# Optimization experiments

Hardware: AMD Instinct MI355X
Metric: run time of the kernel (lower is better)

Reference implementation:

```python
import jax, jax.numpy as jnp
import numpy as np

B, S, H, R = 4, 1024, 1024, 32


def setup_inputs() -> dict:
    key = jax.random.key(0)
    k1, k2, k3 = jax.random.split(key, 3)
    hidden_states = jax.random.normal(k1, (B, S, H), dtype=jnp.float32)
    # full cartesian grid of (seq_idx, hidden_idx), as required by the final
    # out.view(B, S, H, 1) reshape in the original module
    n = jnp.arange(S * H, dtype=jnp.int64)
    all_indices = jnp.stack([n // H, n % H], axis=1)  # [S*H, 2]
    # Linear weights, torch layout [out_features, in_features], scaled like kaiming-uniform-ish
    seq_W = jax.random.normal(k2, (R, H), dtype=jnp.float32) / np.sqrt(H)
    hid_W = jax.random.normal(k3, (R, S), dtype=jnp.float32) / np.sqrt(S)
    cp_weight = jnp.ones((1, R), dtype=jnp.float32)  # frozen all-ones CP mixing weight
    return {"hidden_states": hidden_states, "all_indices": all_indices,
            "seq_W": seq_W, "hid_W": hid_W, "cp_weight": cp_weight}


def reference(hidden_states, all_indices, seq_W, hid_W, cp_weight):
    # seq-mode factor: Linear(H -> R) over [B, S, H] -> [B, S, R]
    seq_emb = jnp.einsum('bsh,rh->bsr', hidden_states, seq_W)
    # hidden-mode factor: Linear(S -> R) over transposed [B, H, S] -> [B, H, R]
    hid_emb = jnp.einsum('bsh,rs->bhr', hidden_states, hid_W)
    s_idx = all_indices[:, 0]  # [N]
    h_idx = all_indices[:, 1]  # [N]
    g_seq = seq_emb[:, s_idx, :]  # [B, N, R] gather along seq axis
    g_hid = hid_emb[:, h_idx, :]  # [B, N, R] gather along hidden axis
    # hadamard + rank reduction with (frozen) CP weight; out_units == 1 squeezed
    out = jnp.einsum('bnr,bnr,r->bn', g_seq, g_hid, cp_weight[0])
    return out.reshape(B, S, H)
```

## Files before the change

### kernel.cpp

```cpp
#include <hip/hip_runtime.h>

typedef __attribute__((ext_vector_type(8))) short bf16x8;
typedef __attribute__((ext_vector_type(4))) float f32x4;
typedef __attribute__((ext_vector_type(2))) float f32x2;

__device__ __forceinline__ short f2bf(float x) {
    union { float f; unsigned u; } v; v.f = x;
    unsigned r = v.u + 0x7FFFu + ((v.u >> 16) & 1u);
    return (short)(r >> 16);
}

__global__ __launch_bounds__(256) void gemm_fused(
    const float* __restrict__ hs, const float* __restrict__ seqW,
    const float* __restrict__ hidW, float* __restrict__ E )
{
    __shared__ float red[4][16][32];

    const int bid = blockIdx.x;
    const bool hid = bid >= 256;
    const int mt  = hid ? bid - 256 : bid;
    const int tid = threadIdx.x;
    const int wv  = tid >> 6;
    const int l   = tid & 63;
    const int l15 = l & 15;
    const int g   = l >> 4;
    const int m0  = mt * 16;
    const int mrow = m0 + l15;

    const float* __restrict__ W = hid ? hidW : seqW;
    size_t arow;
    if (hid) arow = ((size_t)(mrow >> 10) << 20) + (size_t)(mrow & 1023);
    else     arow = (size_t)mrow << 10;

    f32x4 acc0 = {0.f,0.f,0.f,0.f}, acc1 = {0.f,0.f,0.f,0.f};
    const int kbase = wv * 256;

    for (int ks = 0; ks < 8; ++ks) {
        const int kb = kbase + ks * 32 + g * 8;
        bf16x8 af, bf0, bf1;
        if (hid) {
            const float* pa = hs + arow + (size_t)kb * 1024;
            #pragma unroll
            for (int j = 0; j < 8; ++j) af[j] = f2bf(pa[(size_t)j * 1024]);
        } else {
            const f32x4* pa = (const f32x4*)(hs + arow + kb);
            f32x4 a0 = pa[0], a1 = pa[1];
            af[0]=f2bf(a0.x); af[1]=f2bf(a0.y); af[2]=f2bf(a0.z); af[3]=f2bf(a0.w);
            af[4]=f2bf(a1.x); af[5]=f2bf(a1.y); af[6]=f2bf(a1.z); af[7]=f2bf(a1.w);
        }
        {
            const f32x4* pb = (const f32x4*)(W + (size_t)l15 * 1024 + kb);
            f32x4 b0 = pb[0], b1 = pb[1];
            bf0[0]=f2bf(b0.x); bf0[1]=f2bf(b0.y); bf0[2]=f2bf(b0.z); bf0[3]=f2bf(b0.w);
            bf0[4]=f2bf(b1.x); bf0[5]=f2bf(b1.y); bf0[6]=f2bf(b1.z); bf0[7]=f2bf(b1.w);
        }
        {
            const f32x4* pb = (const f32x4*)(W + (size_t)(l15 + 16) * 1024 + kb);
            f32x4 b0 = pb[0], b1 = pb[1];
            bf1[0]=f2bf(b0.x); bf1[1]=f2bf(b0.y); bf1[2]=f2bf(b0.z); bf1[3]=f2bf(b0.w);
            bf1[4]=f2bf(b1.x); bf1[5]=f2bf(b1.y); bf1[6]=f2bf(b1.z); bf1[7]=f2bf(b1.w);
        }
        acc0 = __builtin_amdgcn_mfma_f32_16x16x32_bf16(af, bf0, acc0, 0, 0, 0);
        acc1 = __builtin_amdgcn_mfma_f32_16x16x32_bf16(af, bf1, acc1, 0, 0, 0);
    }

    #pragma unroll
    for (int r = 0; r < 4; ++r) {
        red[wv][4 * g + r][l15]      = acc0[r];
        red[wv][4 * g + r][l15 + 16] = acc1[r];
    }
    __syncthreads();

    const int o = tid * 2;
    const float* rf = &red[0][0][0];
    f32x2 v;
    v.x = rf[o]     + rf[512 + o]     + rf[1024 + o]     + rf[1536 + o];
    v.y = rf[o + 1] + rf[512 + o + 1] + rf[1024 + o + 1] + rf[1536 + o + 1];
    float* Eo = E + (hid ? (size_t)4096 * 32 : 0) + (size_t)m0 * 32 + o;
    *(f32x2*)Eo = v;
}

__global__ __launch_bounds__(256) void k3(const float* __restrict__ SeqE,
                                          const float* __restrict__ HidE,
                                          const float* __restrict__ cpw,
                                          float* __restrict__ out)
{
    __shared__ float s_w[32][36];
    __shared__ float s_h[64][36];
    const int tid = threadIdx.x;
    const int b  = blockIdx.z;
    const int s0 = blockIdx.x * 32;
    const int h0 = blockIdx.y * 64;

    {
        const int si = tid >> 3;
        const int r4 = (tid & 7) * 4;
        f32x4 v  = *(const f32x4*)(SeqE + ((size_t)(b * 1024 + s0 + si)) * 32 + r4);
        f32x4 wv = *(const f32x4*)(cpw + r4);
        v *= wv;
        *(f32x4*)&s_w[si][r4] = v;
    }
    #pragma unroll
    for (int t = 0; t < 2; ++t) {
        const int fi = tid + t * 256;
        const int hx = fi >> 3;
        const int r4 = (fi & 7) * 4;
        f32x4 v = *(const f32x4*)(HidE + ((size_t)(b * 1024 + h0 + hx)) * 32 + r4);
        *(f32x4*)&s_h[hx][r4] = v;
    }
    __syncthreads();

    const int hx = tid & 63;
    const int sg = tid >> 6;
    float hv[32];
    #pragma unroll
    for (int r4 = 0; r4 < 32; r4 += 4) {
        f32x4 v = *(const f32x4*)&s_h[hx][r4];
        hv[r4] = v.x; hv[r4+1] = v.y; hv[r4+2] = v.z; hv[r4+3] = v.w;
    }
    float res[8];
    #pragma unroll
    for (int si = 0; si < 8; ++si) {
        const int s = sg * 8 + si;
        float acc = 0.f;
        #pragma unroll
        for (int r4 = 0; r4 < 32; r4 += 4) {
            f32x4 v = *(const f32x4*)&s_w[s][r4];
            acc += v.x * hv[r4] + v.y * hv[r4+1] + v.z * hv[r4+2] + v.w * hv[r4+3];
        }
        res[si] = acc;
    }
    #pragma unroll
    for (int si = 0; si < 8; ++si) {
        const int s = s0 + sg * 8 + si;
        out[((size_t)(b * 1024 + s)) * 1024 + h0 + hx] = res[si];
    }
}

extern "C" void kernel_launch(void* const* d_in, const int* in_sizes, int n_in,
                              void* d_out, int out_size, void* d_ws, size_t ws_size,
                              hipStream_t stream) {
    const float* hs   = (const float*)d_in[0];
    const float* seqW = (const float*)d_in[2];
    const float* hidW = (const float*)d_in[3];
    const float* cpw  = (const float*)d_in[4];
    float* out = (float*)d_out;

    float* E = (float*)d_ws;

    gemm_fused<<<512, 256, 0, stream>>>(hs, seqW, hidW, E);
    dim3 grid3(32, 16, 4);
    k3<<<grid3, 256, 0, stream>>>(E, E + (size_t)4096 * 32, cpw, out);
}
```

Baseline: 25.56 us.

## Split GEMM K dimension into four chunks and reduce partials in consumer kernel

The factor GEMM kernel now launches four times as many blocks, each covering a quarter of the K range, and writes partial results to four workspace slices. The rank-product kernel sums the four partial slices as it loads its tiles. The aim is more parallelism and shorter per-block latency on a GPU with many CUs, where 512 blocks underfill the machine. In exchange the workspace traffic grows fourfold and the second kernel does more global loads.

```diff
diff --git a/kernel.cpp b/kernel.cpp
--- a/kernel.cpp
+++ b/kernel.cpp
@@ -12,13 +12,15 @@
 
 __global__ __launch_bounds__(256) void gemm_fused(
     const float* __restrict__ hs, const float* __restrict__ seqW,
-    const float* __restrict__ hidW, float* __restrict__ E )
+    const float* __restrict__ hidW, float* __restrict__ P )
 {
     __shared__ float red[4][16][32];
 
-    const int bid = blockIdx.x;
-    const bool hid = bid >= 256;
-    const int mt  = hid ? bid - 256 : bid;
+    const int bid   = blockIdx.x;
+    const int tile  = bid >> 2;
+    const int kchunk = bid & 3;
+    const bool hid  = tile >= 256;
+    const int mt    = hid ? tile - 256 : tile;
     const int tid = threadIdx.x;
     const int wv  = tid >> 6;
     const int l   = tid & 63;
@@ -33,9 +35,10 @@
     else     arow = (size_t)mrow << 10;
 
     f32x4 acc0 = {0.f,0.f,0.f,0.f}, acc1 = {0.f,0.f,0.f,0.f};
-    const int kbase = wv * 256;
+    const int kbase = kchunk * 256 + wv * 64;
 
-    for (int ks = 0; ks < 8; ++ks) {
+    #pragma unroll
+    for (int ks = 0; ks < 2; ++ks) {
         const int kb = kbase + ks * 32 + g * 8;
         bf16x8 af, bf0, bf1;
         if (hid) {
@@ -76,12 +79,13 @@
     f32x2 v;
     v.x = rf[o]     + rf[512 + o]     + rf[1024 + o]     + rf[1536 + o];
     v.y = rf[o + 1] + rf[512 + o + 1] + rf[1024 + o + 1] + rf[1536 + o + 1];
-    float* Eo = E + (hid ? (size_t)4096 * 32 : 0) + (size_t)m0 * 32 + o;
-    *(f32x2*)Eo = v;
+    float* Po = P + (size_t)kchunk * (2 * 4096 * 32)
+                  + (hid ? (size_t)4096 * 32 : 0)
+                  + (size_t)m0 * 32 + o;
+    *(f32x2*)Po = v;
 }
 
-__global__ __launch_bounds__(256) void k3(const float* __restrict__ SeqE,
-                                          const float* __restrict__ HidE,
+__global__ __launch_bounds__(256) void k3(const float* __restrict__ P,
                                           const float* __restrict__ cpw,
                                           float* __restrict__ out)
 {
@@ -91,11 +95,16 @@
     const int b  = blockIdx.z;
     const int s0 = blockIdx.x * 32;
     const int h0 = blockIdx.y * 64;
+    const size_t CH = (size_t)2 * 4096 * 32;
 
     {
         const int si = tid >> 3;
         const int r4 = (tid & 7) * 4;
-        f32x4 v  = *(const f32x4*)(SeqE + ((size_t)(b * 1024 + s0 + si)) * 32 + r4);
+        const float* base = P + ((size_t)(b * 1024 + s0 + si)) * 32 + r4;
+        f32x4 v = *(const f32x4*)(base)
+                + *(const f32x4*)(base + CH)
+                + *(const f32x4*)(base + 2 * CH)
+                + *(const f32x4*)(base + 3 * CH);
         f32x4 wv = *(const f32x4*)(cpw + r4);
         v *= wv;
         *(f32x4*)&s_w[si][r4] = v;
@@ -105,7 +114,12 @@
         const int fi = tid + t * 256;
         const int hx = fi >> 3;
         const int r4 = (fi & 7) * 4;
-        f32x4 v = *(const f32x4*)(HidE + ((size_t)(b * 1024 + h0 + hx)) * 32 + r4);
+        const float* base = P + (size_t)4096 * 32
+                              + ((size_t)(b * 1024 + h0 + hx)) * 32 + r4;
+        f32x4 v = *(const f32x4*)(base)
+                + *(const f32x4*)(base + CH)
+                + *(const f32x4*)(base + 2 * CH)
+                + *(const f32x4*)(base + 3 * CH);
         *(f32x4*)&s_h[hx][r4] = v;
     }
     __syncthreads();
@@ -146,9 +160,9 @@
     const float* cpw  = (const float*)d_in[4];
     float* out = (float*)d_out;
 
-    float* E = (float*)d_ws;
+    float* P = (float*)d_ws;
 
-    gemm_fused<<<512, 256, 0, stream>>>(hs, seqW, hidW, E);
+    gemm_fused<<<2048, 256, 0, stream>>>(hs, seqW, hidW, P);
     dim3 grid3(32, 16, 4);
-    k3<<<grid3, 256, 0, stream>>>(E, E + (size_t)4096 * 32, cpw, out);
+    k3<<<grid3, 256, 0, stream>>>(P, cpw, out);
 }
```

New measurement: 28.88 us. 13.0% more time.
